# Kernel optimization log

Measured on AMD Instinct MI355X. Metric: run time of the kernel, lower is better.

## Reference

```python
import jax, jax.numpy as jnp
import numpy as np

B, S, D, H, DFF = 2, 2048, 1024, 16, 4096
HD = D // H
EPS = 1e-5


def setup_inputs() -> dict:
    key = jax.random.key(0)
    ks = jax.random.split(key, 8)
    s = lambda fan_in: 1.0 / np.sqrt(fan_in)
    return {
        "x": jax.random.normal(ks[0], (B, S, D), jnp.float32),
        "ln1_g": jnp.ones((D,), jnp.float32),
        "ln1_b": jnp.zeros((D,), jnp.float32),
        "Wq": jax.random.normal(ks[1], (D, D), jnp.float32) * s(D),
        "Wk": jax.random.normal(ks[2], (D, D), jnp.float32) * s(D),
        "Wv": jax.random.normal(ks[3], (D, D), jnp.float32) * s(D),
        "Wo": jax.random.normal(ks[4], (D, D), jnp.float32) * s(D),
        "bo": jnp.zeros((D,), jnp.float32),
        "ln2_g": jnp.ones((D,), jnp.float32),
        "ln2_b": jnp.zeros((D,), jnp.float32),
        "W1": jax.random.normal(ks[5], (D, DFF), jnp.float32) * s(D),
        "b1": jnp.zeros((DFF,), jnp.float32),
        "W2": jax.random.normal(ks[6], (DFF, D), jnp.float32) * s(DFF),
        "b2": jnp.zeros((D,), jnp.float32),
    }


def _layernorm(x, g, b):
    mu = jnp.mean(x, axis=-1, keepdims=True)
    var = jnp.var(x, axis=-1, keepdims=True)
    return (x - mu) * jax.lax.rsqrt(var + EPS) * g + b


def reference(x, ln1_g, ln1_b, Wq, Wk, Wv, Wo, bo, ln2_g, ln2_b, W1, b1, W2, b2):
    # --- pre-LN + causal multi-head attention + residual ---
    h = _layernorm(x, ln1_g, ln1_b)
    q = (h @ Wq).reshape(B, S, H, HD).transpose(0, 2, 1, 3)  # [B,H,S,hd]
    k = (h @ Wk).reshape(B, S, H, HD).transpose(0, 2, 1, 3)
    v = (h @ Wv).reshape(B, S, H, HD).transpose(0, 2, 1, 3)
    scores = jnp.einsum("bhqd,bhkd->bhqk", q, k) / jnp.sqrt(jnp.float32(HD))
    causal = jnp.triu(jnp.ones((S, S), bool), k=1)  # True above diagonal -> masked
    scores = jnp.where(causal, -jnp.inf, scores)
    attn = jax.nn.softmax(scores, axis=-1)  # dropout is identity at inference
    ctx = jnp.einsum("bhqk,bhkd->bhqd", attn, v)
    ctx = ctx.transpose(0, 2, 1, 3).reshape(B, S, D)
    x = x + ctx @ Wo + bo
    # --- pre-LN + MLP + residual ---
    h = _layernorm(x, ln2_g, ln2_b)
    h = jax.nn.gelu(h @ W1 + b1, approximate=False)  # torch nn.GELU default = exact
    x = x + h @ W2 + b2
    return x
```

## Files before the change

kernel.cpp:

```cpp
#include <hip/hip_runtime.h>
#include <hip/hip_bf16.h>
#include <math.h>

using bf16 = __hip_bfloat16;
typedef short bf16x8 __attribute__((ext_vector_type(8)));
typedef float f32x4 __attribute__((ext_vector_type(4)));

static constexpr int B = 2, S = 2048, D = 1024, H = 16, HD = 64, DFF = 4096;
static constexpr int NR = B * S;
static constexpr int DQ = 3072;
static constexpr float EPS = 1e-5f;

__device__ __forceinline__ bf16 f2b(float v) { return __float2bfloat16(v); }

typedef __attribute__((address_space(1))) const void* gp1_t;
typedef __attribute__((address_space(3))) void* sp3_t;
__device__ __forceinline__ void gld_lds16(const bf16* g, bf16* l) {
    __builtin_amdgcn_global_load_lds((gp1_t)(const void*)g, (sp3_t)(void*)l, 16, 0, 0);
}

__device__ __forceinline__ void convT_body(const float* __restrict__ src,
                                           bf16* __restrict__ dst,
                                           int K, int N, int k0, int n0, int tid) {
    __shared__ float tile[64][65];
    const int r = tid >> 4, c = (tid & 15) * 4;
#pragma unroll
    for (int rr = 0; rr < 64; rr += 16) {
        float4 v = *(const float4*)&src[(size_t)(k0 + r + rr) * N + n0 + c];
        tile[r + rr][c] = v.x; tile[r + rr][c + 1] = v.y;
        tile[r + rr][c + 2] = v.z; tile[r + rr][c + 3] = v.w;
    }
    __syncthreads();
    const int n = tid >> 2, ks = (tid & 3) * 16;
    union { bf16 h[16]; int4 v2[2]; } o;
#pragma unroll
    for (int i = 0; i < 16; ++i) o.h[i] = f2b(tile[ks + i][n]);
    bf16* dp = &dst[(size_t)(n0 + n) * K + k0 + ks];
    *(int4*)dp = o.v2[0];
    *(int4*)(dp + 8) = o.v2[1];
}

__global__ __launch_bounds__(256) void convT_kernel(const float* __restrict__ src,
                                                    bf16* __restrict__ dst,
                                                    int K, int N) {
    convT_body(src, dst, K, N, blockIdx.x * 64, blockIdx.y * 64, threadIdx.x);
}

__global__ __launch_bounds__(256) void convT5_kernel(const float* __restrict__ Wq,
                                                     const float* __restrict__ Wk,
                                                     const float* __restrict__ Wv,
                                                     const float* __restrict__ Wo,
                                                     const float* __restrict__ W2,
                                                     bf16* __restrict__ WqkvT,
                                                     bf16* __restrict__ WoT,
                                                     bf16* __restrict__ W2T) {
    const int bid = blockIdx.x;
    const float* src;
    bf16* dst;
    int K, N, bx, by;
    if (bid < 768) {
        const int j = bid >> 8, r = bid & 255;
        src = (j == 0) ? Wq : ((j == 1) ? Wk : Wv);
        dst = WqkvT + (size_t)j * D * D;
        K = D; N = D; bx = r & 15; by = r >> 4;
    } else if (bid < 1024) {
        const int r = bid - 768;
        src = Wo; dst = WoT; K = D; N = D; bx = r & 15; by = r >> 4;
    } else {
        const int r = bid - 1024;
        src = W2; dst = W2T; K = DFF; N = D; bx = r & 63; by = r >> 6;
    }
    convT_body(src, dst, K, N, bx * 64, by * 64, threadIdx.x);
}

__global__ __launch_bounds__(256) void ln_kernel(const float* __restrict__ x,
                                                 const float* __restrict__ g,
                                                 const float* __restrict__ b,
                                                 bf16* __restrict__ out) {
    const int row = blockIdx.x;
    const int tid = threadIdx.x;
    const float4 v4 = ((const float4*)(x + (size_t)row * D))[tid];
    float v[4] = {v4.x, v4.y, v4.z, v4.w};
    float s = v[0] + v[1] + v[2] + v[3];
    float sq = v[0] * v[0] + v[1] * v[1] + v[2] * v[2] + v[3] * v[3];
#pragma unroll
    for (int off = 32; off >= 1; off >>= 1) {
        s += __shfl_xor(s, off);
        sq += __shfl_xor(sq, off);
    }
    __shared__ float ssum[4], ssq[4];
    const int wave = tid >> 6;
    if ((tid & 63) == 0) { ssum[wave] = s; ssq[wave] = sq; }
    __syncthreads();
    s = ssum[0] + ssum[1] + ssum[2] + ssum[3];
    sq = ssq[0] + ssq[1] + ssq[2] + ssq[3];
    const float mu = s * (1.0f / D);
    const float var = sq * (1.0f / D) - mu * mu;
    const float rstd = rsqrtf(var + EPS);
    bf16* orow = out + (size_t)row * D;
#pragma unroll
    for (int i = 0; i < 4; ++i) {
        const int c = tid * 4 + i;
        orow[c] = f2b((v[i] - mu) * rstd * g[c] + b[c]);
    }
}

template <int EPI, int BN, int TPB>
__global__ __launch_bounds__(256) void gemm_bt(const bf16* __restrict__ A,
                                               const bf16* __restrict__ Bt,
                                               const float* __restrict__ bias,
                                               const float* __restrict__ res,
                                               void* __restrict__ Cv,
                                               int M, int N, int K) {
    constexpr int NTW = BN / 32;
    constexpr int ASZ = 128 * 32, BSZ = BN * 32;
    constexpr int CST = BN + 8;
    __shared__ __align__(16) bf16 smem[2 * (ASZ + BSZ)];

    const int Mtiles = M / 128;
    const int p = blockIdx.x;
    const int tm = p % Mtiles;
    const int tn0 = (p / Mtiles) * TPB;
    const int tid = threadIdx.x;
    const int wave = tid >> 6, lane = tid & 63;
    const int wm = wave >> 1, wn = wave & 1;
    const int quad = lane >> 4, l16 = lane & 15;

    const int s_row = tid >> 2, s_seg = (tid & 3) * 8;
    const size_t K64 = (size_t)64 * K;
    const int nk = K / 32;

    for (int tp = 0; tp < TPB; ++tp) {
        const int tn = tn0 + tp;
        if (tp) __syncthreads();

        f32x4 acc[4][NTW];
#pragma unroll
        for (int i = 0; i < 4; ++i)
#pragma unroll
            for (int j = 0; j < NTW; ++j) acc[i][j] = (f32x4){0.f, 0.f, 0.f, 0.f};

        const bf16* Ap = A + (size_t)(tm * 128 + s_row) * K + s_seg;
        const bf16* Bp = Bt + (size_t)(tn * BN + s_row) * K + s_seg;

        gld_lds16(Ap, smem + tid * 8);
        gld_lds16(Ap + K64, smem + (256 + tid) * 8);
        gld_lds16(Bp, smem + 2 * ASZ + tid * 8);
        if constexpr (BN == 128) gld_lds16(Bp + K64, smem + 2 * ASZ + (256 + tid) * 8);
        Ap += 32;
        Bp += 32;

        for (int kt = 0; kt < nk; ++kt) {
            const int cur = kt & 1, nxt = cur ^ 1;
            bf16* Acur = smem + cur * ASZ;
            bf16* Bcur = smem + 2 * ASZ + cur * BSZ;
            __syncthreads();
            if (kt + 1 < nk) {
                bf16* Anxt = smem + nxt * ASZ;
                bf16* Bnxt = smem + 2 * ASZ + nxt * BSZ;
                gld_lds16(Ap, Anxt + tid * 8);
                gld_lds16(Ap + K64, Anxt + (256 + tid) * 8);
                gld_lds16(Bp, Bnxt + tid * 8);
                if constexpr (BN == 128) gld_lds16(Bp + K64, Bnxt + (256 + tid) * 8);
                Ap += 32;
                Bp += 32;
            }

            bf16x8 aF[4], bF[NTW];
#pragma unroll
            for (int mt = 0; mt < 4; ++mt)
                aF[mt] = *(const bf16x8*)(Acur + (wm * 64 + mt * 16 + l16) * 32 + quad * 8);
#pragma unroll
            for (int nt = 0; nt < NTW; ++nt)
                bF[nt] = *(const bf16x8*)(Bcur + (wn * (BN / 2) + nt * 16 + l16) * 32 + quad * 8);
#pragma unroll
            for (int mt = 0; mt < 4; ++mt)
#pragma unroll
                for (int nt = 0; nt < NTW; ++nt)
                    acc[mt][nt] = __builtin_amdgcn_mfma_f32_16x16x32_bf16(
                        aF[mt], bF[nt], acc[mt][nt], 0, 0, 0);
        }

        if constexpr (EPI == 1) {
#pragma unroll
            for (int nt = 0; nt < NTW; ++nt) {
                const int col = tn * BN + wn * (BN / 2) + nt * 16 + l16;
                const float bv = bias[col];
#pragma unroll
                for (int mt = 0; mt < 4; ++mt) {
                    const int row0 = tm * 128 + wm * 64 + mt * 16 + quad * 4;
#pragma unroll
                    for (int j = 0; j < 4; ++j) {
                        const size_t idx = (size_t)(row0 + j) * N + col;
                        ((float*)Cv)[idx] = acc[mt][nt][j] + bv + res[idx];
                    }
                }
            }
        } else {
            bf16* C = (bf16*)Cv;
            bf16* sm2 = smem;
#pragma unroll
            for (int hh = 0; hh < 2; ++hh) {
                __syncthreads();
                if (wm == hh) {
#pragma unroll
                    for (int nt = 0; nt < NTW; ++nt) {
                        const int ccol = wn * (BN / 2) + nt * 16 + l16;
                        float bv = 0.f;
                        if (EPI == 2) bv = bias[tn * BN + ccol];
#pragma unroll
                        for (int mt = 0; mt < 4; ++mt) {
                            const int r0 = mt * 16 + quad * 4;
#pragma unroll
                            for (int j = 0; j < 4; ++j) {
                                float v = acc[mt][nt][j];
                                if (EPI == 2) {
                                    v += bv;
                                    v = 0.5f * v * (1.0f + erff(v * 0.70710678118654752f));
                                }
                                sm2[(r0 + j) * CST + ccol] = f2b(v);
                            }
                        }
                    }
                }
                __syncthreads();
                bf16* crow = C + (size_t)(tm * 128 + hh * 64) * N + tn * BN;
#pragma unroll
                for (int i = 0; i < BN / 32; ++i) {
                    const int gid = i * 256 + tid;
                    const int row = gid / (BN / 8), c8 = gid % (BN / 8);
                    const int4 val = *(const int4*)(sm2 + row * CST + c8 * 8);
                    *(int4*)(crow + (size_t)row * N + c8 * 8) = val;
                }
            }
        }
    }
}

__global__ __launch_bounds__(256) void fattn_kernel(const bf16* __restrict__ QKV,
                                                    bf16* __restrict__ ctx) {
    const int id = blockIdx.x;
    const int bh = id & 31;
    const int k = id >> 5;
    const int t = (k < 16) ? 31 - k : k - 16;
    const int b = bh >> 4, h = bh & (H - 1);
    const int tid = threadIdx.x;
    const int wave = tid >> 6, lane = tid & 63;
    const int quad = lane >> 4, l16 = lane & 15;
    const bf16* Qp = QKV + (size_t)b * S * DQ + h * HD;
    const bf16* Kp = Qp + D;
    const bf16* Vp = Qp + 2 * D;

    __shared__ __align__(16) bf16 Ks[2][64 * 64];
    __shared__ __align__(16) bf16 Vt[2][64][72];

    const int keyA = tid >> 3;
    const int sA = (keyA & 3) | ((keyA >> 1) & 4);
    const int dsA = ((tid & 7) ^ sA) * 8;
    const size_t K32 = (size_t)32 * DQ;

    const int q0 = t * 64;
    const bf16* qg = Qp + (size_t)(q0 + wave * 16 + l16) * DQ + quad * 8;
    union U8 { bf16 h[8]; bf16x8 v; };
    U8 uq0, uq1;
    uq0.v = *(const bf16x8*)(qg);
    uq1.v = *(const bf16x8*)(qg + 32);
#pragma unroll
    for (int i = 0; i < 8; ++i) {
        uq0.h[i] = f2b(__bfloat162float(uq0.h[i]) * 0.125f);
        uq1.h[i] = f2b(__bfloat162float(uq1.h[i]) * 0.125f);
    }
    const bf16x8 aQ0 = uq0.v;
    const bf16x8 aQ1 = uq1.v;

    const int kb = (l16 >> 2) * 8 + (l16 & 3);
    const int sQ = (l16 & 3) | (((l16 >> 2) & 1) << 2);
    const int ofs0 = kb * 64 + ((quad ^ sQ) * 8);
    const int ofs1 = kb * 64 + (((4 + quad) ^ sQ) * 8);

    f32x4 O[4];
#pragma unroll
    for (int nt = 0; nt < 4; ++nt) O[nt] = (f32x4){0.f, 0.f, 0.f, 0.f};
    float rowm = -3.0e38f, rowl = 0.f;

    gld_lds16(Kp + (size_t)keyA * DQ + dsA, Ks[0] + tid * 8);
    gld_lds16(Kp + K32 + (size_t)keyA * DQ + dsA, Ks[0] + (256 + tid) * 8);
    {
        const bf16* vg = Vp + (size_t)lane * DQ + wave * 16;
        U8 u0, u1;
        u0.v = *(const bf16x8*)vg;
        u1.v = *(const bf16x8*)(vg + 8);
#pragma unroll
        for (int i = 0; i < 8; ++i) {
            Vt[0][wave * 16 + i][lane] = u0.h[i];
            Vt[0][wave * 16 + 8 + i][lane] = u1.h[i];
        }
    }

    const int nch = t + 1;
    for (int c = 0; c < nch; ++c) {
        const int cur = c & 1, nxt = cur ^ 1;
        __syncthreads();
        U8 u0, u1;
        if (c + 1 < nch) {
            const bf16* kg = Kp + (size_t)((c + 1) * 64 + keyA) * DQ + dsA;
            gld_lds16(kg, Ks[nxt] + tid * 8);
            gld_lds16(kg + K32, Ks[nxt] + (256 + tid) * 8);
            const bf16* vg = Vp + (size_t)((c + 1) * 64 + lane) * DQ + wave * 16;
            u0.v = *(const bf16x8*)vg;
            u1.v = *(const bf16x8*)(vg + 8);
        }

        f32x4 sc[4];
        __builtin_amdgcn_s_setprio(1);
#pragma unroll
        for (int m = 0; m < 4; ++m) {
            const bf16* kr = Ks[cur] + (m & 1) * 256 + (m >> 1) * 2048;
            const bf16x8 bK0 = *(const bf16x8*)(kr + ofs0);
            const bf16x8 bK1 = *(const bf16x8*)(kr + ofs1);
            f32x4 z = (f32x4){0.f, 0.f, 0.f, 0.f};
            z = __builtin_amdgcn_mfma_f32_16x16x32_bf16(bK0, aQ0, z, 0, 0, 0);
            z = __builtin_amdgcn_mfma_f32_16x16x32_bf16(bK1, aQ1, z, 0, 0, 0);
            sc[m] = z;
        }
        __builtin_amdgcn_s_setprio(0);
        if (c == nch - 1) {
            const int qloc = wave * 16 + l16;
#pragma unroll
            for (int m = 0; m < 4; ++m) {
                const int kk = quad * 8 + (m & 1) * 4 + (m >> 1) * 32;
#pragma unroll
                for (int j = 0; j < 4; ++j)
                    if (kk + j > qloc) sc[m][j] = -3.0e38f;
            }
        }
        f32x4 mv;
#pragma unroll
        for (int j = 0; j < 4; ++j)
            mv[j] = fmaxf(fmaxf(sc[0][j], sc[1][j]), fmaxf(sc[2][j], sc[3][j]));
        float mx = fmaxf(fmaxf(mv[0], mv[1]), fmaxf(mv[2], mv[3]));
        mx = fmaxf(mx, __shfl_xor(mx, 16));
        mx = fmaxf(mx, __shfl_xor(mx, 32));
        const float mn = fmaxf(rowm, mx);
        const float alq = __expf(rowm - mn);
        rowm = mn;
        float rs = 0.f;
#pragma unroll
        for (int m = 0; m < 4; ++m)
#pragma unroll
            for (int j = 0; j < 4; ++j) {
                sc[m][j] = __expf(sc[m][j] - mn);
                rs += sc[m][j];
            }
        rs += __shfl_xor(rs, 16);
        rs += __shfl_xor(rs, 32);
        rowl = rowl * alq + rs;

        U8 p0, p1;
#pragma unroll
        for (int j = 0; j < 4; ++j) {
            p0.h[j]     = f2b(sc[0][j]);
            p0.h[4 + j] = f2b(sc[1][j]);
            p1.h[j]     = f2b(sc[2][j]);
            p1.h[4 + j] = f2b(sc[3][j]);
        }
#pragma unroll
        for (int nt = 0; nt < 4; ++nt)
#pragma unroll
            for (int j = 0; j < 4; ++j) O[nt][j] *= alq;
        __builtin_amdgcn_s_setprio(1);
#pragma unroll
        for (int nt = 0; nt < 4; ++nt) {
            const bf16x8 bV0 = *(const bf16x8*)&Vt[cur][nt * 16 + l16][quad * 8];
            const bf16x8 bV1 = *(const bf16x8*)&Vt[cur][nt * 16 + l16][32 + quad * 8];
            O[nt] = __builtin_amdgcn_mfma_f32_16x16x32_bf16(bV0, p0.v, O[nt], 0, 0, 0);
            O[nt] = __builtin_amdgcn_mfma_f32_16x16x32_bf16(bV1, p1.v, O[nt], 0, 0, 0);
        }
        __builtin_amdgcn_s_setprio(0);
        if (c + 1 < nch) {
#pragma unroll
            for (int i = 0; i < 8; ++i) {
                Vt[nxt][wave * 16 + i][lane] = u0.h[i];
                Vt[nxt][wave * 16 + 8 + i][lane] = u1.h[i];
            }
        }
    }

    const float rlq = 1.0f / rowl;
    bf16* crow = ctx + (size_t)b * S * D + h * HD + (size_t)(q0 + wave * 16 + l16) * D;
#pragma unroll
    for (int nt = 0; nt < 4; ++nt) {
        union { bf16 h[4]; int2 v; } o;
#pragma unroll
        for (int j = 0; j < 4; ++j) o.h[j] = f2b(O[nt][j] * rlq);
        *(int2*)(crow + nt * 16 + quad * 4) = o.v;
    }
}

extern "C" void kernel_launch(void* const* d_in, const int* in_sizes, int n_in,
                              void* d_out, int out_size, void* d_ws, size_t ws_size,
                              hipStream_t stream) {
    const float* x     = (const float*)d_in[0];
    const float* ln1_g = (const float*)d_in[1];
    const float* ln1_b = (const float*)d_in[2];
    const float* Wq    = (const float*)d_in[3];
    const float* Wk    = (const float*)d_in[4];
    const float* Wv    = (const float*)d_in[5];
    const float* Wo    = (const float*)d_in[6];
    const float* bo    = (const float*)d_in[7];
    const float* ln2_g = (const float*)d_in[8];
    const float* ln2_b = (const float*)d_in[9];
    const float* W1    = (const float*)d_in[10];
    const float* b1    = (const float*)d_in[11];
    const float* W2    = (const float*)d_in[12];
    const float* b2    = (const float*)d_in[13];
    float* out = (float*)d_out;

    char* ws = (char*)d_ws;
    const size_t MB = (size_t)1 << 20;
    bf16* h     = (bf16*)(ws + 0 * MB);
    bf16* W1T   = (bf16*)(ws + 0 * MB);
    bf16* QKVb  = (bf16*)(ws + 8 * MB);
    bf16* hff   = (bf16*)(ws + 8 * MB);
    bf16* ctx   = (bf16*)(ws + 32 * MB);
    bf16* h2    = (bf16*)(ws + 40 * MB);
    bf16* WqkvT = (bf16*)(ws + 48 * MB);
    bf16* WoT   = (bf16*)(ws + 54 * MB);
    bf16* W2T   = (bf16*)(ws + 56 * MB);

    convT5_kernel<<<2048, 256, 0, stream>>>(Wq, Wk, Wv, Wo, W2, WqkvT, WoT, W2T);
    ln_kernel<<<NR, 256, 0, stream>>>(x, ln1_g, ln1_b, h);
    gemm_bt<0, 128, 1><<<(NR / 128) * (DQ / 128), 256, 0, stream>>>(
        h, WqkvT, nullptr, nullptr, QKVb, NR, DQ, D);
    convT_kernel<<<dim3(16, 64), 256, 0, stream>>>(W1, W1T, D, DFF);
    fattn_kernel<<<dim3((S / 64) * B * H), 256, 0, stream>>>(QKVb, ctx);
    gemm_bt<1, 64, 1><<<(NR / 128) * (D / 64), 256, 0, stream>>>(
        ctx, WoT, bo, x, out, NR, D, D);
    ln_kernel<<<NR, 256, 0, stream>>>(out, ln2_g, ln2_b, h2);
    gemm_bt<2, 128, 1><<<(NR / 128) * (DFF / 128), 256, 0, stream>>>(
        h2, W1T, b1, nullptr, hff, NR, DFF, D);
    gemm_bt<1, 64, 1><<<(NR / 128) * (D / 64), 256, 0, stream>>>(
        hff, W2T, b2, out, out, NR, D, DFF);
}
```

Baseline: 373.8 us.

## Add 256x256-tile 8-wave GEMM for QKV and FFN1 projections

Adds a new GEMM kernel that uses 256x256 output tiles, 512 threads and BK=64. It double-buffers XOR-swizzled LDS tiles loaded through global_load_lds, interleaves barriers with MFMA phases and raises wave priority during the MFMA bursts. The QKV projection and the GELU FFN1 projection now use it, and the old bf16 epilogue is removed from gemm_bt. The intent is higher data reuse and better overlap of loads with compute. The cost is higher LDS and register pressure, and fewer blocks (192 and 256), which may underfill the GPU's CUs.

```diff
diff --git a/kernel.cpp b/kernel.cpp
--- a/kernel.cpp
+++ b/kernel.cpp
@@ -105,6 +105,138 @@
     }
 }
 
+template <int EPI>
+__global__ __launch_bounds__(512) void gemm8p(const bf16* __restrict__ A,
+                                              const bf16* __restrict__ Bt,
+                                              const float* __restrict__ bias,
+                                              bf16* __restrict__ C,
+                                              int M, int N, int K) {
+    constexpr int TSZ = 256 * 64;
+    __shared__ __align__(16) bf16 smem[4 * TSZ];
+
+    const int Mtiles = M / 256;
+    const int p = blockIdx.x;
+    const int tm = p % Mtiles;
+    const int tn = p / Mtiles;
+    const int tid = threadIdx.x;
+    const int wave = tid >> 6, lane = tid & 63;
+    const int wr = wave >> 2, wc = wave & 3;
+    const int quad = lane >> 4, l16 = lane & 15;
+
+    const int row0 = tid >> 3;
+    const int g = (tid & 7) ^ (row0 & 7);
+    const bf16* pA = A + (size_t)(tm * 256 + row0) * K + g * 8;
+    const bf16* pB = Bt + (size_t)(tn * 256 + row0) * K + g * 8;
+    const size_t K64 = (size_t)64 * K;
+
+    const int l7 = l16 & 7;
+    const int sk0 = (quad ^ l7) * 8;
+    const int sk1 = ((4 + quad) ^ l7) * 8;
+    const int aoff = (wr * 128 + l16) * 64;
+    const int boff = (wc * 64 + l16) * 64;
+
+    f32x4 acc[8][4];
+#pragma unroll
+    for (int i = 0; i < 8; ++i)
+#pragma unroll
+        for (int j = 0; j < 4; ++j) acc[i][j] = (f32x4){0.f, 0.f, 0.f, 0.f};
+
+    auto stage = [&](int kt, int d) {
+        const bf16* sa = pA + kt * 64;
+        const bf16* sb = pB + kt * 64;
+        bf16* da = smem + d * 2 * TSZ + tid * 8;
+        bf16* db = da + TSZ;
+#pragma unroll
+        for (int i = 0; i < 4; ++i) {
+            gld_lds16(sa + i * K64, da + i * 4096);
+            gld_lds16(sb + i * K64, db + i * 4096);
+        }
+    };
+
+    stage(0, 0);
+    asm volatile("s_waitcnt vmcnt(0)" ::: "memory");
+    __builtin_amdgcn_s_barrier();
+
+    const int nk = K / 64;
+    for (int kt = 0; kt < nk; ++kt) {
+        const int cur = kt & 1;
+        const bf16* Ab = smem + cur * 2 * TSZ;
+        const bf16* Bb = Ab + TSZ;
+        bf16x8 bF[4][2];
+#pragma unroll
+        for (int q = 0; q < 4; ++q) {
+            bf16x8 aF[2][2];
+#pragma unroll
+            for (int x = 0; x < 2; ++x) {
+                const bf16* ar = Ab + aoff + (q * 2 + x) * 1024;
+                aF[x][0] = *(const bf16x8*)(ar + sk0);
+                aF[x][1] = *(const bf16x8*)(ar + sk1);
+            }
+            if (q == 0) {
+#pragma unroll
+                for (int nt = 0; nt < 4; ++nt) {
+                    const bf16* br = Bb + boff + nt * 1024;
+                    bF[nt][0] = *(const bf16x8*)(br + sk0);
+                    bF[nt][1] = *(const bf16x8*)(br + sk1);
+                }
+                if (kt + 1 < nk) stage(kt + 1, cur ^ 1);
+            }
+            __builtin_amdgcn_s_barrier();
+            asm volatile("s_waitcnt lgkmcnt(0)" ::: "memory");
+            __builtin_amdgcn_sched_barrier(0);
+            __builtin_amdgcn_s_setprio(1);
+#pragma unroll
+            for (int x = 0; x < 2; ++x)
+#pragma unroll
+                for (int nt = 0; nt < 4; ++nt) {
+                    acc[q * 2 + x][nt] = __builtin_amdgcn_mfma_f32_16x16x32_bf16(
+                        aF[x][0], bF[nt][0], acc[q * 2 + x][nt], 0, 0, 0);
+                    acc[q * 2 + x][nt] = __builtin_amdgcn_mfma_f32_16x16x32_bf16(
+                        aF[x][1], bF[nt][1], acc[q * 2 + x][nt], 0, 0, 0);
+                }
+            __builtin_amdgcn_s_setprio(0);
+            __builtin_amdgcn_sched_barrier(0);
+            if (q == 3) asm volatile("s_waitcnt vmcnt(0)" ::: "memory");
+            __builtin_amdgcn_s_barrier();
+        }
+    }
+
+#pragma unroll
+    for (int hh = 0; hh < 2; ++hh) {
+        __syncthreads();
+        if (wr == hh) {
+#pragma unroll
+            for (int nt = 0; nt < 4; ++nt) {
+                const int ccol = wc * 64 + nt * 16 + l16;
+                float bv = 0.f;
+                if (EPI == 2) bv = bias[tn * 256 + ccol];
+#pragma unroll
+                for (int mt = 0; mt < 8; ++mt) {
+                    const int r0 = mt * 16 + quad * 4;
+#pragma unroll
+                    for (int j = 0; j < 4; ++j) {
+                        float v = acc[mt][nt][j];
+                        if (EPI == 2) {
+                            v += bv;
+                            v = 0.5f * v * (1.0f + erff(v * 0.70710678118654752f));
+                        }
+                        smem[(r0 + j) * 264 + ccol] = f2b(v);
+                    }
+                }
+            }
+        }
+        __syncthreads();
+        bf16* crow = C + (size_t)(tm * 256 + hh * 128) * N + tn * 256;
+#pragma unroll
+        for (int i = 0; i < 8; ++i) {
+            const int gid = i * 512 + tid;
+            const int row = gid >> 5, c8 = gid & 31;
+            const int4 val = *(const int4*)(smem + row * 264 + c8 * 8);
+            *(int4*)(crow + (size_t)row * N + c8 * 8) = val;
+        }
+    }
+}
+
 template <int EPI, int BN, int TPB>
 __global__ __launch_bounds__(256) void gemm_bt(const bf16* __restrict__ A,
                                                const bf16* __restrict__ Bt,
@@ -114,7 +246,6 @@
                                                int M, int N, int K) {
     constexpr int NTW = BN / 32;
     constexpr int ASZ = 128 * 32, BSZ = BN * 32;
-    constexpr int CST = BN + 8;
     __shared__ __align__(16) bf16 smem[2 * (ASZ + BSZ)];
 
     const int Mtiles = M / 128;
@@ -181,56 +312,17 @@
                         aF[mt], bF[nt], acc[mt][nt], 0, 0, 0);
         }
 
-        if constexpr (EPI == 1) {
-#pragma unroll
-            for (int nt = 0; nt < NTW; ++nt) {
-                const int col = tn * BN + wn * (BN / 2) + nt * 16 + l16;
-                const float bv = bias[col];
-#pragma unroll
-                for (int mt = 0; mt < 4; ++mt) {
-                    const int row0 = tm * 128 + wm * 64 + mt * 16 + quad * 4;
-#pragma unroll
-                    for (int j = 0; j < 4; ++j) {
-                        const size_t idx = (size_t)(row0 + j) * N + col;
-                        ((float*)Cv)[idx] = acc[mt][nt][j] + bv + res[idx];
-                    }
-                }
-            }
-        } else {
-            bf16* C = (bf16*)Cv;
-            bf16* sm2 = smem;
-#pragma unroll
-            for (int hh = 0; hh < 2; ++hh) {
-                __syncthreads();
-                if (wm == hh) {
-#pragma unroll
-                    for (int nt = 0; nt < NTW; ++nt) {
-                        const int ccol = wn * (BN / 2) + nt * 16 + l16;
-                        float bv = 0.f;
-                        if (EPI == 2) bv = bias[tn * BN + ccol];
-#pragma unroll
-                        for (int mt = 0; mt < 4; ++mt) {
-                            const int r0 = mt * 16 + quad * 4;
-#pragma unroll
-                            for (int j = 0; j < 4; ++j) {
-                                float v = acc[mt][nt][j];
-                                if (EPI == 2) {
-                                    v += bv;
-                                    v = 0.5f * v * (1.0f + erff(v * 0.70710678118654752f));
-                                }
-                                sm2[(r0 + j) * CST + ccol] = f2b(v);
-                            }
-                        }
-                    }
-                }
-                __syncthreads();
-                bf16* crow = C + (size_t)(tm * 128 + hh * 64) * N + tn * BN;
-#pragma unroll
-                for (int i = 0; i < BN / 32; ++i) {
-                    const int gid = i * 256 + tid;
-                    const int row = gid / (BN / 8), c8 = gid % (BN / 8);
-                    const int4 val = *(const int4*)(sm2 + row * CST + c8 * 8);
-                    *(int4*)(crow + (size_t)row * N + c8 * 8) = val;
+#pragma unroll
+        for (int nt = 0; nt < NTW; ++nt) {
+            const int col = tn * BN + wn * (BN / 2) + nt * 16 + l16;
+            const float bv = bias[col];
+#pragma unroll
+            for (int mt = 0; mt < 4; ++mt) {
+                const int row0 = tm * 128 + wm * 64 + mt * 16 + quad * 4;
+#pragma unroll
+                for (int j = 0; j < 4; ++j) {
+                    const size_t idx = (size_t)(row0 + j) * N + col;
+                    ((float*)Cv)[idx] = acc[mt][nt][j] + bv + res[idx];
                 }
             }
         }
@@ -430,15 +522,15 @@
 
     convT5_kernel<<<2048, 256, 0, stream>>>(Wq, Wk, Wv, Wo, W2, WqkvT, WoT, W2T);
     ln_kernel<<<NR, 256, 0, stream>>>(x, ln1_g, ln1_b, h);
-    gemm_bt<0, 128, 1><<<(NR / 128) * (DQ / 128), 256, 0, stream>>>(
-        h, WqkvT, nullptr, nullptr, QKVb, NR, DQ, D);
+    gemm8p<0><<<(NR / 256) * (DQ / 256), 512, 0, stream>>>(
+        h, WqkvT, nullptr, QKVb, NR, DQ, D);
     convT_kernel<<<dim3(16, 64), 256, 0, stream>>>(W1, W1T, D, DFF);
     fattn_kernel<<<dim3((S / 64) * B * H), 256, 0, stream>>>(QKVb, ctx);
     gemm_bt<1, 64, 1><<<(NR / 128) * (D / 64), 256, 0, stream>>>(
         ctx, WoT, bo, x, out, NR, D, D);
     ln_kernel<<<NR, 256, 0, stream>>>(out, ln2_g, ln2_b, h2);
-    gemm_bt<2, 128, 1><<<(NR / 128) * (DFF / 128), 256, 0, stream>>>(
-        h2, W1T, b1, nullptr, hff, NR, DFF, D);
+    gemm8p<2><<<(NR / 256) * (DFF / 256), 512, 0, stream>>>(
+        h2, W1T, b1, hff, NR, DFF, D);
     gemm_bt<1, 64, 1><<<(NR / 128) * (D / 64), 256, 0, stream>>>(
         hff, W2T, b2, out, out, NR, D, DFF);
 }
```

Result: slower. 562.1 us (+50.4%).

## Double GEMM K-step to 64 and use 64-wide N tiles for all GEMMs

Applied to the files above, without the earlier changes.

The bf16 GEMM now stages 64 K elements per double-buffered step as two 32-wide halves, halving the number of block barriers per K. The QKV and FFN1 GEMMs switch from 128-wide to 64-wide N tiles, doubling block count for more parallelism but increasing A-tile re-reads. The bf16 epilogue now stages the full 128-row tile through shared memory in one pass instead of two halves.

```diff
diff --git a/kernel.cpp b/kernel.cpp
--- a/kernel.cpp
+++ b/kernel.cpp
@@ -113,7 +113,9 @@
                                                void* __restrict__ Cv,
                                                int M, int N, int K) {
     constexpr int NTW = BN / 32;
-    constexpr int ASZ = 128 * 32, BSZ = BN * 32;
+    constexpr int AHALF = 128 * 32;
+    constexpr int BHALF = BN * 32;
+    constexpr int ASZ = 2 * AHALF, BSZ = 2 * BHALF;
     constexpr int CST = BN + 8;
     __shared__ __align__(16) bf16 smem[2 * (ASZ + BSZ)];
 
@@ -126,9 +128,9 @@
     const int wm = wave >> 1, wn = wave & 1;
     const int quad = lane >> 4, l16 = lane & 15;
 
-    const int s_row = tid >> 2, s_seg = (tid & 3) * 8;
+    const int r4 = tid >> 2, s4 = (tid & 3) * 8;
     const size_t K64 = (size_t)64 * K;
-    const int nk = K / 32;
+    const int nk = K / 64;
 
     for (int tp = 0; tp < TPB; ++tp) {
         const int tn = tn0 + tp;
@@ -140,15 +142,17 @@
 #pragma unroll
             for (int j = 0; j < NTW; ++j) acc[i][j] = (f32x4){0.f, 0.f, 0.f, 0.f};
 
-        const bf16* Ap = A + (size_t)(tm * 128 + s_row) * K + s_seg;
-        const bf16* Bp = Bt + (size_t)(tn * BN + s_row) * K + s_seg;
+        const bf16* Ap = A + (size_t)(tm * 128 + r4) * K + s4;
+        const bf16* Bp = Bt + (size_t)(tn * BN + r4) * K + s4;
 
         gld_lds16(Ap, smem + tid * 8);
         gld_lds16(Ap + K64, smem + (256 + tid) * 8);
+        gld_lds16(Ap + 32, smem + (512 + tid) * 8);
+        gld_lds16(Ap + K64 + 32, smem + (768 + tid) * 8);
         gld_lds16(Bp, smem + 2 * ASZ + tid * 8);
-        if constexpr (BN == 128) gld_lds16(Bp + K64, smem + 2 * ASZ + (256 + tid) * 8);
-        Ap += 32;
-        Bp += 32;
+        gld_lds16(Bp + 32, smem + 2 * ASZ + (256 + tid) * 8);
+        Ap += 64;
+        Bp += 64;
 
         for (int kt = 0; kt < nk; ++kt) {
             const int cur = kt & 1, nxt = cur ^ 1;
@@ -160,25 +164,32 @@
                 bf16* Bnxt = smem + 2 * ASZ + nxt * BSZ;
                 gld_lds16(Ap, Anxt + tid * 8);
                 gld_lds16(Ap + K64, Anxt + (256 + tid) * 8);
+                gld_lds16(Ap + 32, Anxt + (512 + tid) * 8);
+                gld_lds16(Ap + K64 + 32, Anxt + (768 + tid) * 8);
                 gld_lds16(Bp, Bnxt + tid * 8);
-                if constexpr (BN == 128) gld_lds16(Bp + K64, Bnxt + (256 + tid) * 8);
-                Ap += 32;
-                Bp += 32;
-            }
-
-            bf16x8 aF[4], bF[NTW];
-#pragma unroll
-            for (int mt = 0; mt < 4; ++mt)
-                aF[mt] = *(const bf16x8*)(Acur + (wm * 64 + mt * 16 + l16) * 32 + quad * 8);
-#pragma unroll
-            for (int nt = 0; nt < NTW; ++nt)
-                bF[nt] = *(const bf16x8*)(Bcur + (wn * (BN / 2) + nt * 16 + l16) * 32 + quad * 8);
-#pragma unroll
-            for (int mt = 0; mt < 4; ++mt)
+                gld_lds16(Bp + 32, Bnxt + (256 + tid) * 8);
+                Ap += 64;
+                Bp += 64;
+            }
+
+#pragma unroll
+            for (int ks = 0; ks < 2; ++ks) {
+                const bf16* Ah = Acur + ks * AHALF;
+                const bf16* Bh = Bcur + ks * BHALF;
+                bf16x8 aF[4], bF[NTW];
+#pragma unroll
+                for (int mt = 0; mt < 4; ++mt)
+                    aF[mt] = *(const bf16x8*)(Ah + (wm * 64 + mt * 16 + l16) * 32 + quad * 8);
 #pragma unroll
                 for (int nt = 0; nt < NTW; ++nt)
-                    acc[mt][nt] = __builtin_amdgcn_mfma_f32_16x16x32_bf16(
-                        aF[mt], bF[nt], acc[mt][nt], 0, 0, 0);
+                    bF[nt] = *(const bf16x8*)(Bh + (wn * (BN / 2) + nt * 16 + l16) * 32 + quad * 8);
+#pragma unroll
+                for (int mt = 0; mt < 4; ++mt)
+#pragma unroll
+                    for (int nt = 0; nt < NTW; ++nt)
+                        acc[mt][nt] = __builtin_amdgcn_mfma_f32_16x16x32_bf16(
+                            aF[mt], bF[nt], acc[mt][nt], 0, 0, 0);
+            }
         }
 
         if constexpr (EPI == 1) {
@@ -198,40 +209,34 @@
             }
         } else {
             bf16* C = (bf16*)Cv;
-            bf16* sm2 = smem;
-#pragma unroll
-            for (int hh = 0; hh < 2; ++hh) {
-                __syncthreads();
-                if (wm == hh) {
-#pragma unroll
-                    for (int nt = 0; nt < NTW; ++nt) {
-                        const int ccol = wn * (BN / 2) + nt * 16 + l16;
-                        float bv = 0.f;
-                        if (EPI == 2) bv = bias[tn * BN + ccol];
-#pragma unroll
-                        for (int mt = 0; mt < 4; ++mt) {
-                            const int r0 = mt * 16 + quad * 4;
-#pragma unroll
-                            for (int j = 0; j < 4; ++j) {
-                                float v = acc[mt][nt][j];
-                                if (EPI == 2) {
-                                    v += bv;
-                                    v = 0.5f * v * (1.0f + erff(v * 0.70710678118654752f));
-                                }
-                                sm2[(r0 + j) * CST + ccol] = f2b(v);
-                            }
+            __syncthreads();
+#pragma unroll
+            for (int nt = 0; nt < NTW; ++nt) {
+                const int ccol = wn * (BN / 2) + nt * 16 + l16;
+                float bv = 0.f;
+                if (EPI == 2) bv = bias[tn * BN + ccol];
+#pragma unroll
+                for (int mt = 0; mt < 4; ++mt) {
+                    const int r0 = wm * 64 + mt * 16 + quad * 4;
+#pragma unroll
+                    for (int j = 0; j < 4; ++j) {
+                        float v = acc[mt][nt][j];
+                        if (EPI == 2) {
+                            v += bv;
+                            v = 0.5f * v * (1.0f + erff(v * 0.70710678118654752f));
                         }
+                        smem[(r0 + j) * CST + ccol] = f2b(v);
                     }
                 }
-                __syncthreads();
-                bf16* crow = C + (size_t)(tm * 128 + hh * 64) * N + tn * BN;
-#pragma unroll
-                for (int i = 0; i < BN / 32; ++i) {
-                    const int gid = i * 256 + tid;
-                    const int row = gid / (BN / 8), c8 = gid % (BN / 8);
-                    const int4 val = *(const int4*)(sm2 + row * CST + c8 * 8);
-                    *(int4*)(crow + (size_t)row * N + c8 * 8) = val;
-                }
+            }
+            __syncthreads();
+            bf16* crow = C + (size_t)(tm * 128) * N + tn * BN;
+#pragma unroll
+            for (int i = 0; i < BN / 16; ++i) {
+                const int gid = i * 256 + tid;
+                const int row = gid / (BN / 8), c8 = gid % (BN / 8);
+                const int4 val = *(const int4*)(smem + row * CST + c8 * 8);
+                *(int4*)(crow + (size_t)row * N + c8 * 8) = val;
             }
         }
     }
@@ -430,14 +435,14 @@
 
     convT5_kernel<<<2048, 256, 0, stream>>>(Wq, Wk, Wv, Wo, W2, WqkvT, WoT, W2T);
     ln_kernel<<<NR, 256, 0, stream>>>(x, ln1_g, ln1_b, h);
-    gemm_bt<0, 128, 1><<<(NR / 128) * (DQ / 128), 256, 0, stream>>>(
+    gemm_bt<0, 64, 1><<<(NR / 128) * (DQ / 64), 256, 0, stream>>>(
         h, WqkvT, nullptr, nullptr, QKVb, NR, DQ, D);
     convT_kernel<<<dim3(16, 64), 256, 0, stream>>>(W1, W1T, D, DFF);
     fattn_kernel<<<dim3((S / 64) * B * H), 256, 0, stream>>>(QKVb, ctx);
     gemm_bt<1, 64, 1><<<(NR / 128) * (D / 64), 256, 0, stream>>>(
         ctx, WoT, bo, x, out, NR, D, D);
     ln_kernel<<<NR, 256, 0, stream>>>(out, ln2_g, ln2_b, h2);
-    gemm_bt<2, 128, 1><<<(NR / 128) * (DFF / 128), 256, 0, stream>>>(
+    gemm_bt<2, 64, 1><<<(NR / 128) * (DFF / 64), 256, 0, stream>>>(
         h2, W1T, b1, nullptr, hff, NR, DFF, D);
     gemm_bt<1, 64, 1><<<(NR / 128) * (D / 64), 256, 0, stream>>>(
         hff, W2T, b2, out, out, NR, D, DFF);
```

After: 334.4 us. -10.6%, faster.
